# Optimization experiments

Measured on AMD Instinct MI355X. Metric: run time of the kernel, lower is better.

Reference implementation:

```python
import jax, jax.numpy as jnp
import numpy as np

K = 4
EDGE_NUM = 8978
SLOPE = 0.33


def _add_self_loops(ei, w, n):
    # add_self_loops(..., fill_value=-1.0); inputs assumed already coalesced
    loop = jnp.arange(n, dtype=ei.dtype)
    src = jnp.concatenate([ei[0], loop])
    dst = jnp.concatenate([ei[1], loop])
    w = jnp.concatenate([w, jnp.full((n,), -1.0, w.dtype)])
    return src, dst, w


def _cheb_bn_lrelu(x, src, dst, w, theta, bias, gamma, beta):
    # HodgeChebConv (PyG ChebConv recurrence) + BatchNorm + LeakyReLU; dropout = eval/no-op
    n = x.shape[0]

    def prop(z):  # y[dst] += w * z[src]
        return jax.ops.segment_sum(w[:, None] * z[src], dst, num_segments=n)

    Tx0 = x
    out = jnp.einsum('ni,io->no', Tx0, theta[0])
    Tx1 = prop(Tx0)
    out = out + jnp.einsum('ni,io->no', Tx1, theta[1])
    for k in range(2, K):
        Tx2 = 2.0 * prop(Tx1) - Tx0
        out = out + jnp.einsum('ni,io->no', Tx2, theta[k])
        Tx0, Tx1 = Tx1, Tx2
    out = out + bias
    mu = out.mean(0)
    var = out.var(0)
    out = (out - mu) * jax.lax.rsqrt(var + 1e-5) * gamma + beta
    return jnp.where(out >= 0, out, SLOPE * out)


def _bn(x, g, b):
    mu = x.mean(0)
    var = x.var(0)
    return (x - mu) * jax.lax.rsqrt(var + 1e-5) * g + b


def setup_inputs() -> dict:
    key = jax.random.key(0)
    ks = jax.random.split(key, 16)
    f32 = jnp.float32
    B = 64
    N = B * EDGE_NUM
    N2 = N // 2
    E = N * 8
    E1 = N2 * 8
    inp = {}
    inp['x_s'] = jax.random.normal(ks[0], (N, 1), f32)
    inp['edge_index_s'] = jax.random.randint(ks[1], (2, E), 0, N)
    inp['edge_weight_s'] = jax.random.normal(ks[2], (E,), f32) * 0.1
    inp['edge_index_s1'] = jax.random.randint(ks[3], (2, E1), 0, N2)
    inp['edge_weight_s1'] = jax.random.normal(ks[4], (E1,), f32) * 0.1
    # graclus-style pairing of node matchings (deterministic stand-in)
    inp['cluster'] = jnp.arange(N, dtype=jnp.int32) // 2
    inp['theta0'] = jax.random.normal(ks[5], (K, 1, 32), f32) * 0.1
    inp['bias0'] = jnp.zeros((32,), f32)
    inp['gamma0'] = jnp.ones((32,), f32)
    inp['beta0'] = jnp.zeros((32,), f32)
    inp['theta1'] = jax.random.normal(ks[6], (K, 32, 32), f32) * 0.1
    inp['bias1'] = jnp.zeros((32,), f32)
    inp['gamma1'] = jnp.ones((32,), f32)
    inp['beta1'] = jnp.zeros((32,), f32)
    inp['theta2'] = jax.random.normal(ks[7], (K, 32, 1), f32) * 0.1
    inp['bias2'] = jnp.zeros((1,), f32)
    inp['gamma2'] = jnp.ones((1,), f32)
    inp['beta2'] = jnp.zeros((1,), f32)
    LIN_IN = EDGE_NUM // 2  # 4489
    inp['W1'] = jax.random.normal(ks[8], (LIN_IN, 256), f32) * 0.02
    inp['b1'] = jnp.zeros((256,), f32)
    inp['g1'] = jnp.ones((256,), f32)
    inp['be1'] = jnp.zeros((256,), f32)
    inp['W2'] = jax.random.normal(ks[9], (256, 128), f32) * 0.05
    inp['b2'] = jnp.zeros((128,), f32)
    inp['g2'] = jnp.ones((128,), f32)
    inp['be2'] = jnp.zeros((128,), f32)
    inp['W3'] = jax.random.normal(ks[10], (128, 1), f32) * 0.05
    inp['b3'] = jnp.zeros((1,), f32)
    return inp


def reference(x_s, edge_weight_s, edge_weight_s1, theta0, bias0, gamma0, beta0,
              theta1, bias1, gamma1, beta1, theta2, bias2, gamma2, beta2,
              W1, b1, g1, be1, W2, b2, g2, be2, W3, b3,
              edge_index_s, edge_index_s1, cluster):
    n = x_s.shape[0]
    batch = n // EDGE_NUM
    n2 = n // 2
    src, dst, w = _add_self_loops(edge_index_s, edge_weight_s, n)
    x = _cheb_bn_lrelu(x_s, src, dst, w, theta0, bias0, gamma0, beta0)
    # Graclus max-pool with externally supplied cluster assignment + pooled graph
    x = jax.ops.segment_max(x, cluster, num_segments=n2)
    src1, dst1, w1 = _add_self_loops(edge_index_s1, edge_weight_s1, n2)
    x = _cheb_bn_lrelu(x, src1, dst1, w1, theta1, bias1, gamma1, beta1)
    x = _cheb_bn_lrelu(x, src1, dst1, w1, theta2, bias2, gamma2, beta2)
    x = x.reshape(batch, -1)  # [B, edge_num/2] since last channel = 1
    x = jax.nn.relu(_bn(x @ W1 + b1, g1, be1))
    x = jax.nn.relu(_bn(x @ W2 + b2, g2, be2))
    return x @ W3 + b3
```

## Files before the change

### kernel.cpp

```cpp
#include <hip/hip_runtime.h>
#include <hip/hip_fp16.h>

#define TPB 256
#define PBLK 512
#define BSH 12
#define BKT 4096
#define PCH 2048

__global__ __launch_bounds__(256) void bcount_k(const int* __restrict__ dst,
                                                int* __restrict__ bcnt, int NB, int E) {
  __shared__ int h[256];
  int tid = threadIdx.x;
  h[tid] = 0;
  __syncthreads();
  int stride = gridDim.x * 256;
  for (int e = blockIdx.x * 256 + tid; e < E; e += stride) atomicAdd(&h[dst[e] >> BSH], 1);
  __syncthreads();
  if (tid < NB && h[tid]) atomicAdd(&bcnt[tid], h[tid]);
}

__global__ void bscan_k(const int* __restrict__ bcnt, int* __restrict__ bbase,
                        int* __restrict__ bcur, int NB) {
  __shared__ int ls[256];
  int tid = threadIdx.x;
  int v = (tid < NB) ? bcnt[tid] : 0;
  ls[tid] = v;
  __syncthreads();
  for (int off = 1; off < 256; off <<= 1) {
    int t = (tid >= off) ? ls[tid - off] : 0;
    __syncthreads();
    ls[tid] += t;
    __syncthreads();
  }
  if (tid < NB) {
    bbase[tid] = ls[tid] - v;
    bcur[tid] = ls[tid] - v;
  }
}

__global__ __launch_bounds__(256) void bpart_k(const int* __restrict__ src,
                                               const int* __restrict__ dst,
                                               const float* __restrict__ w, int* __restrict__ gcur,
                                               int* __restrict__ psrc, int* __restrict__ pw,
                                               int* __restrict__ pdst, int NB, int E) {
  __shared__ int hist[256], start[256], resv[256], lcur[256];
  __shared__ int s_src[PCH], s_w[PCH], s_dst[PCH];
  __shared__ int total;
  int tid = threadIdx.x;
  int base = blockIdx.x * PCH;
  hist[tid] = 0;
  __syncthreads();
  int es[8], ds[8], wsv[8], bs[8];
#pragma unroll
  for (int i = 0; i < 8; ++i) {
    int e = base + i * 256 + tid;
    bool v = e < E;
    ds[i] = v ? dst[e] : 0;
    es[i] = v ? src[e] : 0;
    wsv[i] = v ? __float_as_int(w[e]) : 0;
    bs[i] = v ? (ds[i] >> BSH) : -1;
    if (v) atomicAdd(&hist[bs[i]], 1);
  }
  __syncthreads();
  int hv = hist[tid];
  start[tid] = hv;
  __syncthreads();
  for (int off = 1; off < 256; off <<= 1) {
    int t = (tid >= off) ? start[tid - off] : 0;
    __syncthreads();
    start[tid] += t;
    __syncthreads();
  }
  int ex = start[tid] - hv;
  __syncthreads();
  start[tid] = ex;
  lcur[tid] = ex;
  if (tid == 255) total = ex + hv;
  if (tid < NB && hv) resv[tid] = atomicAdd(&gcur[tid], hv);
  __syncthreads();
#pragma unroll
  for (int i = 0; i < 8; ++i) {
    if (bs[i] >= 0) {
      int p = atomicAdd(&lcur[bs[i]], 1);
      s_src[p] = es[i];
      s_w[p] = wsv[i];
      s_dst[p] = ds[i];
    }
  }
  __syncthreads();
  int m = total;
  for (int i = tid; i < m; i += 256) {
    int d = s_dst[i];
    int b = d >> BSH;
    int g = resv[b] + (i - start[b]);
    psrc[g] = s_src[i];
    pw[g] = s_w[i];
    pdst[g] = d;
  }
}

__global__ __launch_bounds__(1024) void bbuild_k(const int* __restrict__ psrc,
                                                 const int* __restrict__ pw,
                                                 const int* __restrict__ pdst,
                                                 const int* __restrict__ bbase,
                                                 const int* __restrict__ bcnt,
                                                 int* __restrict__ rowptr, int2* __restrict__ csw,
                                                 int n, int NB, int Etot) {
  __shared__ int hist[BKT];
  __shared__ int cur[BKT];
  __shared__ int aux[1024];
  int tid = threadIdx.x;
  int b = blockIdx.x;
  int node0 = b << BSH;
  int nn = min(BKT, n - node0);
  for (int i = tid; i < BKT; i += 1024) hist[i] = 0;
  __syncthreads();
  int ebase = bbase[b], ecnt = bcnt[b];
  for (int i = tid; i < ecnt; i += 1024) atomicAdd(&hist[pdst[ebase + i] - node0], 1);
  __syncthreads();
  int h0 = hist[tid * 4], h1 = hist[tid * 4 + 1], h2 = hist[tid * 4 + 2], h3 = hist[tid * 4 + 3];
  int s = h0 + h1 + h2 + h3;
  aux[tid] = s;
  __syncthreads();
  for (int off = 1; off < 1024; off <<= 1) {
    int t = (tid >= off) ? aux[tid - off] : 0;
    __syncthreads();
    aux[tid] += t;
    __syncthreads();
  }
  int ex = aux[tid] - s;
  hist[tid * 4] = ex;
  hist[tid * 4 + 1] = ex + h0;
  hist[tid * 4 + 2] = ex + h0 + h1;
  hist[tid * 4 + 3] = ex + h0 + h1 + h2;
  cur[tid * 4] = ex;
  cur[tid * 4 + 1] = ex + h0;
  cur[tid * 4 + 2] = ex + h0 + h1;
  cur[tid * 4 + 3] = ex + h0 + h1 + h2;
  __syncthreads();
  for (int j = tid; j < nn; j += 1024) rowptr[node0 + j] = ebase + hist[j];
  if (b == NB - 1 && tid == 0) rowptr[n] = Etot;
  for (int i = tid; i < ecnt; i += 1024) {
    int d = pdst[ebase + i] - node0;
    int p = atomicAdd(&cur[d], 1);
    csw[ebase + p] = make_int2(psrc[ebase + i], pw[ebase + i]);
  }
}

__global__ __launch_bounds__(256) void gather_s_k(float* __restrict__ out,
                                                  const float* __restrict__ z,
                                                  const float* __restrict__ bsub, float cb,
                                                  const int* __restrict__ rowptr,
                                                  const int2* __restrict__ csw, float scale,
                                                  int n) {
  int t = blockIdx.x * TPB + threadIdx.x;
  int node = t >> 3, q = t & 7;
  if (node >= n) return;
  int beg = rowptr[node], deg = rowptr[node + 1] - beg;
  float part = 0.f;
  for (int jb = 0; jb < deg; jb += 8) {
    int j = jb + q;
    int2 e = csw[beg + (j < deg ? j : 0)];
    int sj = (j < deg) ? e.x : 0;
    float zv = z[sj];
    part += (j < deg) ? __int_as_float(e.y) * zv : 0.f;
  }
  part += __shfl_xor(part, 1, 8);
  part += __shfl_xor(part, 2, 8);
  part += __shfl_xor(part, 4, 8);
  if (q == 0) out[node] = scale * (part - z[node]) + cb * bsub[node];
}

__global__ __launch_bounds__(256) void cheb0_fused_k(float4* __restrict__ out,
                                                     const float* __restrict__ x,
                                                     const float* __restrict__ t1,
                                                     const float* __restrict__ t2,
                                                     const int* __restrict__ rowptr,
                                                     const int2* __restrict__ csw,
                                                     const float* __restrict__ th ,
                                                     const float* __restrict__ bias, int n) {
  int t = blockIdx.x * TPB + threadIdx.x;
  int node = t >> 3, q = t & 7;
  if (node >= n) return;
  int beg = rowptr[node], deg = rowptr[node + 1] - beg;
  float part = 0.f;
  for (int jb = 0; jb < deg; jb += 8) {
    int j = jb + q;
    int2 e = csw[beg + (j < deg ? j : 0)];
    int sj = (j < deg) ? e.x : 0;
    float zv = t2[sj];
    part += (j < deg) ? __int_as_float(e.y) * zv : 0.f;
  }
  part += __shfl_xor(part, 1, 8);
  part += __shfl_xor(part, 2, 8);
  part += __shfl_xor(part, 4, 8);
  float t2n = t2[node], t1n = t1[node], xn = x[node];
  float t3 = 2.f * (part - t2n) - t1n;
  const float4* th4 = (const float4*)th;
  float4 a0 = th4[q], a1 = th4[8 + q], a2 = th4[16 + q], a3 = th4[24 + q];
  float4 b = ((const float4*)bias)[q];
  float4 r;
  r.x = xn * a0.x + t1n * a1.x + t2n * a2.x + t3 * a3.x + b.x;
  r.y = xn * a0.y + t1n * a1.y + t2n * a2.y + t3 * a3.y + b.y;
  r.z = xn * a0.z + t1n * a1.z + t2n * a2.z + t3 * a3.z + b.z;
  r.w = xn * a0.w + t1n * a1.w + t2n * a2.w + t3 * a3.w + b.w;
  out[(size_t)node * 8 + q] = r;
}

__device__ __forceinline__ float4 gather_row8h(const uint2* __restrict__ zh,
                                               const int* __restrict__ rowptr,
                                               const int2* __restrict__ csw, int node, int q) {
  int beg = rowptr[node], deg = rowptr[node + 1] - beg;
  int full = min(deg, 8);
  int2 e = csw[beg + (q < deg ? q : 0)];
  int sj[8];
  float wj[8];
#pragma unroll
  for (int j = 0; j < 8; ++j) {
    int s = __shfl(e.x, j, 8);
    float w = __int_as_float(__shfl(e.y, j, 8));
    sj[j] = (j < full) ? s : 0;
    wj[j] = (j < full) ? w : 0.f;
  }
  uint2 v[8];
#pragma unroll
  for (int j = 0; j < 8; ++j) v[j] = zh[(size_t)sj[j] * 8 + q];
  float4 acc = {0.f, 0.f, 0.f, 0.f};
#pragma unroll
  for (int j = 0; j < 8; ++j) {
    float2 a = __half22float2(*(const __half2*)&v[j].x);
    float2 b = __half22float2(*(const __half2*)&v[j].y);
    acc.x = fmaf(wj[j], a.x, acc.x);
    acc.y = fmaf(wj[j], a.y, acc.y);
    acc.z = fmaf(wj[j], b.x, acc.z);
    acc.w = fmaf(wj[j], b.y, acc.w);
  }
  for (int j = 8; j < deg; ++j) {
    int2 ee = csw[beg + j];
    float w = __int_as_float(ee.y);
    uint2 vv = zh[(size_t)ee.x * 8 + q];
    float2 a = __half22float2(*(const __half2*)&vv.x);
    float2 b = __half22float2(*(const __half2*)&vv.y);
    acc.x = fmaf(w, a.x, acc.x);
    acc.y = fmaf(w, a.y, acc.y);
    acc.z = fmaf(w, b.x, acc.z);
    acc.w = fmaf(w, b.y, acc.w);
  }
  return acc;
}

__device__ __forceinline__ uint2 pack_h4(float4 r) {
  __half2 p0 = __float22half2_rn(make_float2(r.x, r.y));
  __half2 p1 = __float22half2_rn(make_float2(r.z, r.w));
  uint2 o;
  o.x = *(const unsigned int*)&p0;
  o.y = *(const unsigned int*)&p1;
  return o;
}

__global__ __launch_bounds__(256) void gather_v32_k(
    float4* __restrict__ out, uint2* __restrict__ outh, const float4* __restrict__ z,
    const uint2* __restrict__ zh, const float4* __restrict__ bsub, float cb,
    const int* __restrict__ rowptr, const int2* __restrict__ csw, float scale, int n) {
  int t = blockIdx.x * TPB + threadIdx.x;
  int node = t >> 3, q = t & 7;
  if (node >= n) return;
  float4 acc = gather_row8h(zh, rowptr, csw, node, q);
  float4 zn = z[(size_t)node * 8 + q];
  float4 r;
  r.x = scale * (acc.x - zn.x);
  r.y = scale * (acc.y - zn.y);
  r.z = scale * (acc.z - zn.z);
  r.w = scale * (acc.w - zn.w);
  if (cb != 0.f) {
    float4 bs = bsub[(size_t)node * 8 + q];
    r.x = fmaf(cb, bs.x, r.x);
    r.y = fmaf(cb, bs.y, r.y);
    r.z = fmaf(cb, bs.z, r.z);
    r.w = fmaf(cb, bs.w, r.w);
  }
  out[(size_t)node * 8 + q] = r;
  outh[(size_t)node * 8 + q] = pack_h4(r);
}

__global__ __launch_bounds__(256) void cheb32_fused_k(
    float4* __restrict__ out, const float4* __restrict__ x0, const float4* __restrict__ x1,
    const float4* __restrict__ x2, const uint2* __restrict__ x2h,
    const int* __restrict__ rowptr, const int2* __restrict__ csw,
    const float* __restrict__ th , const float* __restrict__ bias, int n) {
  __shared__ float sth[4096];
  __shared__ float sx[4][32][36];
  int tid = threadIdx.x;
  for (int i = tid; i < 4096; i += 256) sth[i] = th[i];
  int t = blockIdx.x * TPB + tid;
  int node = t >> 3, q = t & 7, ln = tid >> 3;
  if (node < n) {
    float4 acc = gather_row8h(x2h, rowptr, csw, node, q);
    float4 tb = x2[(size_t)node * 8 + q];
    float4 ta = x1[(size_t)node * 8 + q];
    float4 xi = x0[(size_t)node * 8 + q];
    float4 tc;
    tc.x = 2.f * (acc.x - tb.x) - ta.x;
    tc.y = 2.f * (acc.y - tb.y) - ta.y;
    tc.z = 2.f * (acc.z - tb.z) - ta.z;
    tc.w = 2.f * (acc.w - tb.w) - ta.w;
    *(float4*)&sx[0][ln][q * 4] = xi;
    *(float4*)&sx[1][ln][q * 4] = ta;
    *(float4*)&sx[2][ln][q * 4] = tb;
    *(float4*)&sx[3][ln][q * 4] = tc;
  }
  __syncthreads();
  if (node < n) {
    float4 r = ((const float4*)bias)[q];
#pragma unroll
    for (int k = 0; k < 4; ++k) {
      const float* xr = sx[k][ln];
      const float* tr = &sth[k * 1024 + q * 4];
#pragma unroll
      for (int i = 0; i < 32; ++i) {
        float xv = xr[i];
        float4 tv = *(const float4*)&tr[i * 32];
        r.x = fmaf(xv, tv.x, r.x);
        r.y = fmaf(xv, tv.y, r.y);
        r.z = fmaf(xv, tv.z, r.z);
        r.w = fmaf(xv, tv.w, r.w);
      }
    }
    out[(size_t)node * 8 + q] = r;
  }
}

__global__ __launch_bounds__(256) void cheb1_fused_k(
    float* __restrict__ out, const float4* __restrict__ x0, const float4* __restrict__ x1,
    const float4* __restrict__ x2, const uint2* __restrict__ x2h,
    const int* __restrict__ rowptr, const int2* __restrict__ csw,
    const float* __restrict__ th , const float* __restrict__ bias, int n) {
  int t = blockIdx.x * TPB + threadIdx.x;
  int node = t >> 3, q = t & 7;
  if (node >= n) return;
  float4 acc = gather_row8h(x2h, rowptr, csw, node, q);
  float4 tb = x2[(size_t)node * 8 + q];
  float4 ta = x1[(size_t)node * 8 + q];
  float4 xi = x0[(size_t)node * 8 + q];
  float4 tc;
  tc.x = 2.f * (acc.x - tb.x) - ta.x;
  tc.y = 2.f * (acc.y - tb.y) - ta.y;
  tc.z = 2.f * (acc.z - tb.z) - ta.z;
  tc.w = 2.f * (acc.w - tb.w) - ta.w;
  const float4* th4 = (const float4*)th;
  float4 h0 = th4[q], h1 = th4[8 + q], h2 = th4[16 + q], h3 = th4[24 + q];
  float p = xi.x * h0.x + xi.y * h0.y + xi.z * h0.z + xi.w * h0.w;
  p += ta.x * h1.x + ta.y * h1.y + ta.z * h1.z + ta.w * h1.w;
  p += tb.x * h2.x + tb.y * h2.y + tb.z * h2.z + tb.w * h2.w;
  p += tc.x * h3.x + tc.y * h3.y + tc.z * h3.z + tc.w * h3.w;
  p += __shfl_xor(p, 1);
  p += __shfl_xor(p, 2);
  p += __shfl_xor(p, 4);
  if (q == 0) out[node] = p + bias[0];
}

__global__ void bnlr_pool_k(float* __restrict__ y, __half* __restrict__ yh,
                            const float* __restrict__ x, const float* __restrict__ mv,
                            const float* __restrict__ g, const float* __restrict__ be, int n2c,
                            float slope) {
  int i = blockIdx.x * TPB + threadIdx.x;
  if (i < n2c) {
    int p = i >> 5, c = i & 31;
    float sc = mv[32 + c] * g[c];
    float sh = be[c] - mv[c] * sc;
    float a = x[(size_t)(2 * p) * 32 + c] * sc + sh;
    float b = x[(size_t)(2 * p + 1) * 32 + c] * sc + sh;
    a = a >= 0.f ? a : slope * a;
    b = b >= 0.f ? b : slope * b;
    float r = fmaxf(a, b);
    y[i] = r;
    yh[i] = __float2half(r);
  }
}

__global__ __launch_bounds__(256) void stats_k(const float* __restrict__ x,
                                               float* __restrict__ partial, int C, int total) {
  float s = 0.f, q = 0.f;
  int stride = gridDim.x * TPB;
  for (int i = blockIdx.x * TPB + threadIdx.x; i < total; i += stride) {
    float v = x[i];
    s += v;
    q += v * v;
  }
  __shared__ float ss[256], sq[256];
  int tid = threadIdx.x;
  ss[tid] = s;
  sq[tid] = q;
  __syncthreads();
  for (int st = 128; st >= C; st >>= 1) {
    if (tid < st) {
      ss[tid] += ss[tid + st];
      sq[tid] += sq[tid + st];
    }
    __syncthreads();
  }
  if (tid < C) {
    partial[blockIdx.x * 2 * C + tid] = ss[tid];
    partial[blockIdx.x * 2 * C + C + tid] = sq[tid];
  }
}

__global__ __launch_bounds__(1024) void stats_fin_k(const float* __restrict__ partial,
                                                    float* __restrict__ mv, int C, int nblk,
                                                    float invR) {
  __shared__ float ss[1024], sq[1024];
  int tid = threadIdx.x;
  int G = 1024 / C;
  int g = tid / C, c = tid - g * C;
  float s = 0.f, q = 0.f;
  for (int b = g; b < nblk; b += G) {
    s += partial[b * 2 * C + c];
    q += partial[b * 2 * C + C + c];
  }
  ss[tid] = s;
  sq[tid] = q;
  __syncthreads();
  for (int st = 512; st >= C; st >>= 1) {
    if (tid < st) {
      ss[tid] += ss[tid + st];
      sq[tid] += sq[tid + st];
    }
    __syncthreads();
  }
  if (tid < C) {
    float mu = ss[tid] * invR;
    float var = sq[tid] * invR - mu * mu;
    mv[tid] = mu;
    mv[C + tid] = rsqrtf(var + 1e-5f);
  }
}

__global__ void bn_lrelu_k(float* __restrict__ y, __half* __restrict__ yh,
                           const float* __restrict__ mv, const float* __restrict__ g,
                           const float* __restrict__ be, int C, int total, float slope) {
  int i = blockIdx.x * TPB + threadIdx.x;
  if (i < total) {
    int c = i & (C - 1);
    float v = (y[i] - mv[c]) * mv[C + c] * g[c] + be[c];
    v = v >= 0.f ? v : slope * v;
    y[i] = v;
    if (yh) yh[i] = __float2half(v);
  }
}

__global__ void mlp1_init_k(float* __restrict__ h, const float* __restrict__ bias) {
  int i = blockIdx.x * TPB + threadIdx.x;
  h[i] = bias[i & 255];
}

#define MS 32
__global__ __launch_bounds__(256) void mlp1_split_k(const float* __restrict__ x,
                                                    const float* __restrict__ W,
                                                    float* __restrict__ h, int LIN) {
  int bb = blockIdx.x * 8;
  int s = blockIdx.y;
  int chunk = (LIN + MS - 1) / MS;
  int k0 = s * chunk;
  int k1 = min(k0 + chunk, LIN);
  __shared__ float sx[8][144];
  for (int i = threadIdx.x; i < 8 * chunk; i += 256) {
    int r = i / chunk, k = i - r * chunk;
    sx[r][k] = (k0 + k < LIN) ? x[(size_t)(bb + r) * LIN + k0 + k] : 0.f;
  }
  __syncthreads();
  int o = threadIdx.x;
  float acc[8] = {0.f, 0.f, 0.f, 0.f, 0.f, 0.f, 0.f, 0.f};
  for (int k = k0; k < k1; ++k) {
    float wv = W[(size_t)k * 256 + o];
#pragma unroll
    for (int r = 0; r < 8; ++r) acc[r] = fmaf(sx[r][k - k0], wv, acc[r]);
  }
#pragma unroll
  for (int r = 0; r < 8; ++r) unsafeAtomicAdd(&h[(bb + r) * 256 + o], acc[r]);
}

__global__ void bn_relu64_k(float* __restrict__ h, const float* __restrict__ g,
                            const float* __restrict__ be, int C, int R) {
  int c = blockIdx.x * blockDim.x + threadIdx.x;
  if (c < C) {
    float s = 0.f, q = 0.f;
    for (int r = 0; r < R; ++r) {
      float v = h[r * C + c];
      s += v;
      q += v * v;
    }
    float mu = s / R;
    float inv = rsqrtf(q / R - mu * mu + 1e-5f);
    for (int r = 0; r < R; ++r) {
      float v = (h[r * C + c] - mu) * inv * g[c] + be[c];
      h[r * C + c] = v > 0.f ? v : 0.f;
    }
  }
}

__global__ void mlp2_k(const float* __restrict__ x, const float* __restrict__ W,
                       const float* __restrict__ bias, float* __restrict__ h, int IN, int OUT) {
  __shared__ float sx[256];
  int b = blockIdx.x;
  for (int i = threadIdx.x; i < IN; i += blockDim.x) sx[i] = x[b * IN + i];
  __syncthreads();
  int o = threadIdx.x;
  if (o < OUT) {
    float acc = 0.f;
    for (int i = 0; i < IN; ++i) acc = fmaf(sx[i], W[i * OUT + o], acc);
    h[b * OUT + o] = acc + bias[o];
  }
}

__global__ void mlp3_k(const float* __restrict__ x, const float* __restrict__ W,
                       const float* __restrict__ b3, float* __restrict__ out, int IN, int B) {
  int b = threadIdx.x;
  if (b < B) {
    float acc = 0.f;
    for (int i = 0; i < IN; ++i) acc = fmaf(x[b * IN + i], W[i], acc);
    out[b] = acc + b3[0];
  }
}

extern "C" void kernel_launch(void* const* d_in, const int* in_sizes, int n_in, void* d_out,
                              int out_size, void* d_ws, size_t ws_size, hipStream_t stream) {
  const float* x_s = (const float*)d_in[0];
  const int* ei = (const int*)d_in[1];
  const float* ew = (const float*)d_in[2];
  const int* ei1 = (const int*)d_in[3];
  const float* ew1 = (const float*)d_in[4];
  const float* th0 = (const float*)d_in[6];
  const float* cb0 = (const float*)d_in[7];
  const float* g0 = (const float*)d_in[8];
  const float* be0 = (const float*)d_in[9];
  const float* th1 = (const float*)d_in[10];
  const float* cb1 = (const float*)d_in[11];
  const float* g1c = (const float*)d_in[12];
  const float* be1c = (const float*)d_in[13];
  const float* th2 = (const float*)d_in[14];
  const float* cb2 = (const float*)d_in[15];
  const float* g2c = (const float*)d_in[16];
  const float* be2c = (const float*)d_in[17];
  const float* W1 = (const float*)d_in[18];
  const float* mb1 = (const float*)d_in[19];
  const float* mg1 = (const float*)d_in[20];
  const float* mbe1 = (const float*)d_in[21];
  const float* W2 = (const float*)d_in[22];
  const float* mb2 = (const float*)d_in[23];
  const float* mg2 = (const float*)d_in[24];
  const float* mbe2 = (const float*)d_in[25];
  const float* W3 = (const float*)d_in[26];
  const float* mb3 = (const float*)d_in[27];
  float* outp = (float*)d_out;

  const int N = in_sizes[0];
  const int E = in_sizes[2];
  const int N2 = N / 2;
  const int E1 = in_sizes[4];
  const int B = out_size;
  const int LIN = N2 / B;
  const size_t NC = (size_t)N * 32, N2C = (size_t)N2 * 32;

  const int* srcA = ei;
  const int* dstA = ei + E;
  const int* src1 = ei1;
  const int* dst1 = ei1 + E1;

  float* ws = (float*)d_ws;
  float* OUT0 = ws;
  float* X1 = OUT0 + NC;
  float* TA = X1 + N2C;
  float* TB = TA + N2C;
  float* OUT1 = TB + N2C;
  int* deg1 = (int*)(OUT1 + N2C);
  int* rowptr1 = deg1 + N2;
  int2* csw1 = (int2*)(rowptr1 + N2 + 2);
  float* partial = (float*)(csw1 + E1);
  float* mv = partial + PBLK * 64;
  int* bcnt = (int*)(mv + 64);
  int* bbase = bcnt + 256;
  int* bcur = bbase + 256;
  float* h1 = (float*)(bcur + 256);
  float* h2 = h1 + (size_t)B * 256;
  int* psrc = (int*)OUT0;
  int* pw = psrc + E;
  int* pdst = pw + E;
  int2* csw0 = (int2*)X1;
  float* t1 = TA;
  int* rowptr0 = (int*)TA + N;
  float* t2 = TB;
  float* OUT2 = X1;
  uint2* TAh = (uint2*)OUT0;
  uint2* TBh = (uint2*)(OUT0 + N2C / 2);
  uint2* O1h = (uint2*)(OUT0 + N2C);
  __half* X1h = (__half*)TB;

  auto cdiv = [](long long a, long long b) { return (unsigned)((a + b - 1) / b); };
  int NB0 = (int)cdiv(N, BKT), NB1 = (int)cdiv(N2, BKT);

  hipMemsetAsync(bcnt, 0, 256 * 4, stream);
  bcount_k<<<1024, 256, 0, stream>>>(dstA, bcnt, NB0, E);
  bscan_k<<<1, 256, 0, stream>>>(bcnt, bbase, bcur, NB0);
  bpart_k<<<cdiv(E, PCH), 256, 0, stream>>>(srcA, dstA, ew, bcur, psrc, pw, pdst, NB0, E);
  bbuild_k<<<NB0, 1024, 0, stream>>>(psrc, pw, pdst, bbase, bcnt, rowptr0, csw0, N, NB0, E);

  hipMemsetAsync(bcnt, 0, 256 * 4, stream);
  bcount_k<<<1024, 256, 0, stream>>>(dst1, bcnt, NB1, E1);
  bscan_k<<<1, 256, 0, stream>>>(bcnt, bbase, bcur, NB1);
  bpart_k<<<cdiv(E1, PCH), 256, 0, stream>>>(src1, dst1, ew1, bcur, psrc, pw, pdst, NB1, E1);
  bbuild_k<<<NB1, 1024, 0, stream>>>(psrc, pw, pdst, bbase, bcnt, rowptr1, csw1, N2, NB1, E1);

  gather_s_k<<<cdiv((long long)N * 8, TPB), TPB, 0, stream>>>(t1, x_s, x_s, 0.f, rowptr0, csw0,
                                                              1.f, N);
  gather_s_k<<<cdiv((long long)N * 8, TPB), TPB, 0, stream>>>(t2, t1, x_s, -1.f, rowptr0, csw0,
                                                              2.f, N);
  cheb0_fused_k<<<cdiv((long long)N * 8, TPB), TPB, 0, stream>>>((float4*)OUT0, x_s, t1, t2,
                                                                 rowptr0, csw0, th0, cb0, N);
  stats_k<<<PBLK, TPB, 0, stream>>>(OUT0, partial, 32, (int)NC);
  stats_fin_k<<<1, 1024, 0, stream>>>(partial, mv, 32, PBLK, 1.f / N);
  bnlr_pool_k<<<cdiv(N2C, TPB), TPB, 0, stream>>>(X1, X1h, OUT0, mv, g0, be0, (int)N2C, 0.33f);

  unsigned g = cdiv((long long)N2 * 8, TPB);
  gather_v32_k<<<g, TPB, 0, stream>>>((float4*)TA, TAh, (const float4*)X1, (const uint2*)X1h,
                                      (const float4*)X1, 0.f, rowptr1, csw1, 1.f, N2);
  gather_v32_k<<<g, TPB, 0, stream>>>((float4*)TB, TBh, (const float4*)TA, TAh,
                                      (const float4*)X1, -1.f, rowptr1, csw1, 2.f, N2);
  cheb32_fused_k<<<g, TPB, 0, stream>>>((float4*)OUT1, (const float4*)X1, (const float4*)TA,
                                        (const float4*)TB, TBh, rowptr1, csw1, th1, cb1, N2);
  stats_k<<<PBLK, TPB, 0, stream>>>(OUT1, partial, 32, (int)N2C);
  stats_fin_k<<<1, 1024, 0, stream>>>(partial, mv, 32, PBLK, 1.f / N2);
  bn_lrelu_k<<<cdiv(N2C, TPB), TPB, 0, stream>>>(OUT1, (__half*)O1h, mv, g1c, be1c, 32, (int)N2C,
                                                 0.33f);

  gather_v32_k<<<g, TPB, 0, stream>>>((float4*)TA, TAh, (const float4*)OUT1, O1h,
                                      (const float4*)OUT1, 0.f, rowptr1, csw1, 1.f, N2);
  gather_v32_k<<<g, TPB, 0, stream>>>((float4*)TB, TBh, (const float4*)TA, TAh,
                                      (const float4*)OUT1, -1.f, rowptr1, csw1, 2.f, N2);
  cheb1_fused_k<<<g, TPB, 0, stream>>>(OUT2, (const float4*)OUT1, (const float4*)TA,
                                       (const float4*)TB, TBh, rowptr1, csw1, th2, cb2, N2);
  stats_k<<<PBLK, TPB, 0, stream>>>(OUT2, partial, 1, N2);
  stats_fin_k<<<1, 1024, 0, stream>>>(partial, mv, 1, PBLK, 1.f / N2);
  bn_lrelu_k<<<cdiv(N2, TPB), TPB, 0, stream>>>(OUT2, (__half*)nullptr, mv, g2c, be2c, 1, N2,
                                                0.33f);

  mlp1_init_k<<<cdiv((long long)B * 256, TPB), TPB, 0, stream>>>(h1, mb1);
  mlp1_split_k<<<dim3(B / 8, MS), 256, 0, stream>>>(OUT2, W1, h1, LIN);
  bn_relu64_k<<<1, 256, 0, stream>>>(h1, mg1, mbe1, 256, B);
  mlp2_k<<<B, 128, 0, stream>>>(h1, W2, mb2, h2, 256, 128);
  bn_relu64_k<<<1, 128, 0, stream>>>(h2, mg2, mbe2, 128, B);
  mlp3_k<<<1, 64, 0, stream>>>(h2, W3, mb3, outp, 128, B);
}
```

Baseline: 1.098 ms.

## Store intermediate Chebyshev features only in fp16, dropping fp32 copies

```diff
diff --git a/kernel.cpp b/kernel.cpp
--- a/kernel.cpp
+++ b/kernel.cpp
@@ -207,6 +207,20 @@
   out[(size_t)node * 8 + q] = r;
 }
 
+__device__ __forceinline__ float4 unpack_h4(uint2 u) {
+  float2 a = __half22float2(*(const __half2*)&u.x);
+  float2 b = __half22float2(*(const __half2*)&u.y);
+  return make_float4(a.x, a.y, b.x, b.y);
+}
+__device__ __forceinline__ uint2 pack_h4(float4 r) {
+  __half2 p0 = __float22half2_rn(make_float2(r.x, r.y));
+  __half2 p1 = __float22half2_rn(make_float2(r.z, r.w));
+  uint2 o;
+  o.x = *(const unsigned int*)&p0;
+  o.y = *(const unsigned int*)&p1;
+  return o;
+}
+
 __device__ __forceinline__ float4 gather_row8h(const uint2* __restrict__ zh,
                                                const int* __restrict__ rowptr,
                                                const int2* __restrict__ csw, int node, int q) {
@@ -228,65 +242,53 @@
   float4 acc = {0.f, 0.f, 0.f, 0.f};
 #pragma unroll
   for (int j = 0; j < 8; ++j) {
-    float2 a = __half22float2(*(const __half2*)&v[j].x);
-    float2 b = __half22float2(*(const __half2*)&v[j].y);
-    acc.x = fmaf(wj[j], a.x, acc.x);
-    acc.y = fmaf(wj[j], a.y, acc.y);
-    acc.z = fmaf(wj[j], b.x, acc.z);
-    acc.w = fmaf(wj[j], b.y, acc.w);
+    float4 f = unpack_h4(v[j]);
+    acc.x = fmaf(wj[j], f.x, acc.x);
+    acc.y = fmaf(wj[j], f.y, acc.y);
+    acc.z = fmaf(wj[j], f.z, acc.z);
+    acc.w = fmaf(wj[j], f.w, acc.w);
   }
   for (int j = 8; j < deg; ++j) {
     int2 ee = csw[beg + j];
     float w = __int_as_float(ee.y);
-    uint2 vv = zh[(size_t)ee.x * 8 + q];
-    float2 a = __half22float2(*(const __half2*)&vv.x);
-    float2 b = __half22float2(*(const __half2*)&vv.y);
-    acc.x = fmaf(w, a.x, acc.x);
-    acc.y = fmaf(w, a.y, acc.y);
-    acc.z = fmaf(w, b.x, acc.z);
-    acc.w = fmaf(w, b.y, acc.w);
+    float4 f = unpack_h4(zh[(size_t)ee.x * 8 + q]);
+    acc.x = fmaf(w, f.x, acc.x);
+    acc.y = fmaf(w, f.y, acc.y);
+    acc.z = fmaf(w, f.z, acc.z);
+    acc.w = fmaf(w, f.w, acc.w);
   }
   return acc;
 }
 
-__device__ __forceinline__ uint2 pack_h4(float4 r) {
-  __half2 p0 = __float22half2_rn(make_float2(r.x, r.y));
-  __half2 p1 = __float22half2_rn(make_float2(r.z, r.w));
-  uint2 o;
-  o.x = *(const unsigned int*)&p0;
-  o.y = *(const unsigned int*)&p1;
-  return o;
-}
-
-__global__ __launch_bounds__(256) void gather_v32_k(
-    float4* __restrict__ out, uint2* __restrict__ outh, const float4* __restrict__ z,
-    const uint2* __restrict__ zh, const float4* __restrict__ bsub, float cb,
-    const int* __restrict__ rowptr, const int2* __restrict__ csw, float scale, int n) {
+__global__ __launch_bounds__(256) void gather_v32h_k(uint2* __restrict__ outh,
+                                                     const uint2* __restrict__ zh,
+                                                     const uint2* __restrict__ bsh, float cb,
+                                                     const int* __restrict__ rowptr,
+                                                     const int2* __restrict__ csw, float scale,
+                                                     int n) {
   int t = blockIdx.x * TPB + threadIdx.x;
   int node = t >> 3, q = t & 7;
   if (node >= n) return;
   float4 acc = gather_row8h(zh, rowptr, csw, node, q);
-  float4 zn = z[(size_t)node * 8 + q];
+  float4 zn = unpack_h4(zh[(size_t)node * 8 + q]);
   float4 r;
   r.x = scale * (acc.x - zn.x);
   r.y = scale * (acc.y - zn.y);
   r.z = scale * (acc.z - zn.z);
   r.w = scale * (acc.w - zn.w);
   if (cb != 0.f) {
-    float4 bs = bsub[(size_t)node * 8 + q];
+    float4 bs = unpack_h4(bsh[(size_t)node * 8 + q]);
     r.x = fmaf(cb, bs.x, r.x);
     r.y = fmaf(cb, bs.y, r.y);
     r.z = fmaf(cb, bs.z, r.z);
     r.w = fmaf(cb, bs.w, r.w);
   }
-  out[(size_t)node * 8 + q] = r;
   outh[(size_t)node * 8 + q] = pack_h4(r);
 }
 
 __global__ __launch_bounds__(256) void cheb32_fused_k(
-    float4* __restrict__ out, const float4* __restrict__ x0, const float4* __restrict__ x1,
-    const float4* __restrict__ x2, const uint2* __restrict__ x2h,
-    const int* __restrict__ rowptr, const int2* __restrict__ csw,
+    float4* __restrict__ out, const uint2* __restrict__ x0h, const uint2* __restrict__ x1h,
+    const uint2* __restrict__ x2h, const int* __restrict__ rowptr, const int2* __restrict__ csw,
     const float* __restrict__ th , const float* __restrict__ bias, int n) {
   __shared__ float sth[4096];
   __shared__ float sx[4][32][36];
@@ -296,9 +298,9 @@
   int node = t >> 3, q = t & 7, ln = tid >> 3;
   if (node < n) {
     float4 acc = gather_row8h(x2h, rowptr, csw, node, q);
-    float4 tb = x2[(size_t)node * 8 + q];
-    float4 ta = x1[(size_t)node * 8 + q];
-    float4 xi = x0[(size_t)node * 8 + q];
+    float4 tb = unpack_h4(x2h[(size_t)node * 8 + q]);
+    float4 ta = unpack_h4(x1h[(size_t)node * 8 + q]);
+    float4 xi = unpack_h4(x0h[(size_t)node * 8 + q]);
     float4 tc;
     tc.x = 2.f * (acc.x - tb.x) - ta.x;
     tc.y = 2.f * (acc.y - tb.y) - ta.y;
@@ -331,17 +333,16 @@
 }
 
 __global__ __launch_bounds__(256) void cheb1_fused_k(
-    float* __restrict__ out, const float4* __restrict__ x0, const float4* __restrict__ x1,
-    const float4* __restrict__ x2, const uint2* __restrict__ x2h,
-    const int* __restrict__ rowptr, const int2* __restrict__ csw,
+    float* __restrict__ out, const uint2* __restrict__ x0h, const uint2* __restrict__ x1h,
+    const uint2* __restrict__ x2h, const int* __restrict__ rowptr, const int2* __restrict__ csw,
     const float* __restrict__ th , const float* __restrict__ bias, int n) {
   int t = blockIdx.x * TPB + threadIdx.x;
   int node = t >> 3, q = t & 7;
   if (node >= n) return;
   float4 acc = gather_row8h(x2h, rowptr, csw, node, q);
-  float4 tb = x2[(size_t)node * 8 + q];
-  float4 ta = x1[(size_t)node * 8 + q];
-  float4 xi = x0[(size_t)node * 8 + q];
+  float4 tb = unpack_h4(x2h[(size_t)node * 8 + q]);
+  float4 ta = unpack_h4(x1h[(size_t)node * 8 + q]);
+  float4 xi = unpack_h4(x0h[(size_t)node * 8 + q]);
   float4 tc;
   tc.x = 2.f * (acc.x - tb.x) - ta.x;
   tc.y = 2.f * (acc.y - tb.y) - ta.y;
@@ -359,10 +360,9 @@
   if (q == 0) out[node] = p + bias[0];
 }
 
-__global__ void bnlr_pool_k(float* __restrict__ y, __half* __restrict__ yh,
-                            const float* __restrict__ x, const float* __restrict__ mv,
-                            const float* __restrict__ g, const float* __restrict__ be, int n2c,
-                            float slope) {
+__global__ void bnlr_pool_k(__half* __restrict__ yh, const float* __restrict__ x,
+                            const float* __restrict__ mv, const float* __restrict__ g,
+                            const float* __restrict__ be, int n2c, float slope) {
   int i = blockIdx.x * TPB + threadIdx.x;
   if (i < n2c) {
     int p = i >> 5, c = i & 31;
@@ -372,9 +372,7 @@
     float b = x[(size_t)(2 * p + 1) * 32 + c] * sc + sh;
     a = a >= 0.f ? a : slope * a;
     b = b >= 0.f ? b : slope * b;
-    float r = fmaxf(a, b);
-    y[i] = r;
-    yh[i] = __float2half(r);
+    yh[i] = __float2half(fmaxf(a, b));
   }
 }
 
@@ -443,8 +441,10 @@
     int c = i & (C - 1);
     float v = (y[i] - mv[c]) * mv[C + c] * g[c] + be[c];
     v = v >= 0.f ? v : slope * v;
-    y[i] = v;
-    if (yh) yh[i] = __float2half(v);
+    if (yh)
+      yh[i] = __float2half(v);
+    else
+      y[i] = v;
   }
 }
 
@@ -589,11 +589,11 @@
   float* t1 = TA;
   int* rowptr0 = (int*)TA + N;
   float* t2 = TB;
+  uint2* X1h = (uint2*)X1;
+  uint2* TAh = (uint2*)TA;
+  uint2* TBh = (uint2*)TB;
+  uint2* O1h = (uint2*)OUT0;
   float* OUT2 = X1;
-  uint2* TAh = (uint2*)OUT0;
-  uint2* TBh = (uint2*)(OUT0 + N2C / 2);
-  uint2* O1h = (uint2*)(OUT0 + N2C);
-  __half* X1h = (__half*)TB;
 
   auto cdiv = [](long long a, long long b) { return (unsigned)((a + b - 1) / b); };
   int NB0 = (int)cdiv(N, BKT), NB1 = (int)cdiv(N2, BKT);
@@ -618,26 +618,22 @@
                                                                  rowptr0, csw0, th0, cb0, N);
   stats_k<<<PBLK, TPB, 0, stream>>>(OUT0, partial, 32, (int)NC);
   stats_fin_k<<<1, 1024, 0, stream>>>(partial, mv, 32, PBLK, 1.f / N);
-  bnlr_pool_k<<<cdiv(N2C, TPB), TPB, 0, stream>>>(X1, X1h, OUT0, mv, g0, be0, (int)N2C, 0.33f);
+  bnlr_pool_k<<<cdiv(N2C, TPB), TPB, 0, stream>>>((__half*)X1h, OUT0, mv, g0, be0, (int)N2C,
+                                                  0.33f);
 
   unsigned g = cdiv((long long)N2 * 8, TPB);
-  gather_v32_k<<<g, TPB, 0, stream>>>((float4*)TA, TAh, (const float4*)X1, (const uint2*)X1h,
-                                      (const float4*)X1, 0.f, rowptr1, csw1, 1.f, N2);
-  gather_v32_k<<<g, TPB, 0, stream>>>((float4*)TB, TBh, (const float4*)TA, TAh,
-                                      (const float4*)X1, -1.f, rowptr1, csw1, 2.f, N2);
-  cheb32_fused_k<<<g, TPB, 0, stream>>>((float4*)OUT1, (const float4*)X1, (const float4*)TA,
-                                        (const float4*)TB, TBh, rowptr1, csw1, th1, cb1, N2);
+  gather_v32h_k<<<g, TPB, 0, stream>>>(TAh, X1h, X1h, 0.f, rowptr1, csw1, 1.f, N2);
+  gather_v32h_k<<<g, TPB, 0, stream>>>(TBh, TAh, X1h, -1.f, rowptr1, csw1, 2.f, N2);
+  cheb32_fused_k<<<g, TPB, 0, stream>>>((float4*)OUT1, X1h, TAh, TBh, rowptr1, csw1, th1, cb1,
+                                        N2);
   stats_k<<<PBLK, TPB, 0, stream>>>(OUT1, partial, 32, (int)N2C);
   stats_fin_k<<<1, 1024, 0, stream>>>(partial, mv, 32, PBLK, 1.f / N2);
   bn_lrelu_k<<<cdiv(N2C, TPB), TPB, 0, stream>>>(OUT1, (__half*)O1h, mv, g1c, be1c, 32, (int)N2C,
                                                  0.33f);
 
-  gather_v32_k<<<g, TPB, 0, stream>>>((float4*)TA, TAh, (const float4*)OUT1, O1h,
-                                      (const float4*)OUT1, 0.f, rowptr1, csw1, 1.f, N2);
-  gather_v32_k<<<g, TPB, 0, stream>>>((float4*)TB, TBh, (const float4*)TA, TAh,
-                                      (const float4*)OUT1, -1.f, rowptr1, csw1, 2.f, N2);
-  cheb1_fused_k<<<g, TPB, 0, stream>>>(OUT2, (const float4*)OUT1, (const float4*)TA,
-                                       (const float4*)TB, TBh, rowptr1, csw1, th2, cb2, N2);
+  gather_v32h_k<<<g, TPB, 0, stream>>>(TAh, O1h, O1h, 0.f, rowptr1, csw1, 1.f, N2);
+  gather_v32h_k<<<g, TPB, 0, stream>>>(TBh, TAh, O1h, -1.f, rowptr1, csw1, 2.f, N2);
+  cheb1_fused_k<<<g, TPB, 0, stream>>>(OUT2, O1h, TAh, TBh, rowptr1, csw1, th2, cb2, N2);
   stats_k<<<PBLK, TPB, 0, stream>>>(OUT2, partial, 1, N2);
   stats_fin_k<<<1, 1024, 0, stream>>>(partial, mv, 1, PBLK, 1.f / N2);
   bn_lrelu_k<<<cdiv(N2, TPB), TPB, 0, stream>>>(OUT2, (__half*)nullptr, mv, g2c, be2c, 1, N2,
```

After: 1.040 ms. -5.3%, faster.
